# Kernel tuning notes

Hardware: AMD Instinct MI355X
Metric: run time of the kernel (lower is better)

## Reference

```python
import jax, jax.numpy as jnp
import numpy as np

N, D, M = 2048, 1024, 1024


def setup_inputs() -> dict:
    key = jax.random.key(0)
    ks = jax.random.split(key, 10)
    inputs = jax.random.normal(ks[0], (N, D), jnp.float32)
    # topological parent pointers: parent[t] > t; root (t=N-1) points to dummy slot N
    p = jax.random.randint(ks[1], (N,), jnp.arange(1, N + 1), N + 1)
    parent = jnp.where(jnp.arange(N) < N - 1, jnp.minimum(p, N - 1), N)
    s = 0.02
    Wioux = jax.random.normal(ks[2], (3 * M, D), jnp.float32) * s
    bioux = jax.random.normal(ks[3], (3 * M,), jnp.float32) * s
    Wiouh = jax.random.normal(ks[4], (3 * M, M), jnp.float32) * s
    biouh = jax.random.normal(ks[5], (3 * M,), jnp.float32) * s
    Wfx = jax.random.normal(ks[6], (M, D), jnp.float32) * s
    bfx = jax.random.normal(ks[7], (M,), jnp.float32) * s
    Wfh = jax.random.normal(ks[8], (M, M), jnp.float32) * s
    bfh = jax.random.normal(ks[9], (M,), jnp.float32) * s
    return dict(inputs=inputs, parent=parent, Wioux=Wioux, bioux=bioux,
                Wiouh=Wiouh, biouh=biouh, Wfx=Wfx, bfx=bfx, Wfh=Wfh, bfh=bfh)


def reference(inputs, parent, Wioux, bioux, Wiouh, biouh, Wfx, bfx, Wfh, bfh):
    # Child-Sum Tree-LSTM over nodes in topological order (children before parents).
    n, m = inputs.shape[0], Wfx.shape[0]
    ioux_all = inputs @ Wioux.T + bioux              # [N, 3M] self.ioux(inputs) for all nodes
    fx_all = inputs @ Wfx.T + bfx                    # [N, M]  self.fx(inputs) for all nodes
    fx_pad = jnp.concatenate([fx_all, jnp.zeros((1, m), fx_all.dtype)], axis=0)
    fxp = fx_pad[parent]                             # [N, M]  fx of each node's parent

    def step(carry, xs):
        h_sum, fc_sum = carry                        # [N+1, M] accumulated child sums
        t, iou_x, fxp_t, p = xs
        iou = iou_x + h_sum[t] @ Wiouh.T + biouh     # ioux(x) + iouh(child_h_sum)
        i, o, u = jnp.split(iou, 3)
        i, o, u = jax.nn.sigmoid(i), jax.nn.sigmoid(o), jnp.tanh(u)
        c = i * u + fc_sum[t]                        # i*u + sum_k f_k * c_k
        h = o * jnp.tanh(c)
        # forget gate for this node as a child of its parent: sigmoid(fh(h) + fx(x_parent))
        f = jax.nn.sigmoid(h @ Wfh.T + bfh + fxp_t)
        return (h_sum.at[p].add(h), fc_sum.at[p].add(f * c)), (c, h)

    init = (jnp.zeros((n + 1, m), inputs.dtype), jnp.zeros((n + 1, m), inputs.dtype))
    _, (cs, hs) = jax.lax.scan(step, init,
                               (jnp.arange(n), ioux_all, fxp, parent))
    # root is the last node in topological order; torch returns (c, h) each [1, mem_dim]
    return cs[-1:], hs[-1:]
```

## Files before the change

kernel.cpp:

```cpp
#include <hip/hip_runtime.h>

#define NN 2048
#define MD 1024
#define NOUT 4096
#define GBLK 256
#define GTHR 512
#define CAP 1024

typedef __attribute__((ext_vector_type(8))) short short8;
typedef __attribute__((ext_vector_type(4))) float f4;

__device__ __forceinline__ unsigned short f2bf(float f) {
  unsigned u = __float_as_uint(f);
  u += 0x7fffu + ((u >> 16) & 1u);
  return (unsigned short)(u >> 16);
}
__device__ __forceinline__ uint4 pack8(f4 a, f4 b) {
  uint4 r;
  r.x = f2bf(a[0]) | ((unsigned)f2bf(a[1]) << 16);
  r.y = f2bf(a[2]) | ((unsigned)f2bf(a[3]) << 16);
  r.z = f2bf(b[0]) | ((unsigned)f2bf(b[1]) << 16);
  r.w = f2bf(b[2]) | ((unsigned)f2bf(b[3]) << 16);
  return r;
}
__device__ __forceinline__ float blo(unsigned u) { return __uint_as_float(u << 16); }
__device__ __forceinline__ float bhi(unsigned u) { return __uint_as_float(u & 0xffff0000u); }
__device__ __forceinline__ float sigm(float x) { return 1.0f / (1.0f + __expf(-x)); }
__device__ __forceinline__ float tanh_(float x) { return 1.0f - 2.0f / (1.0f + __expf(2.0f * x)); }

__global__ __launch_bounds__(256) void cvt_bf16_kernel(const float* __restrict__ s,
                                                       unsigned short* __restrict__ d, int n4) {
  int i = blockIdx.x * 256 + threadIdx.x;
  if (i < n4) {
    f4 v = *((const f4*)s + i);
    unsigned lo = f2bf(v[0]) | ((unsigned)f2bf(v[1]) << 16);
    unsigned hi = f2bf(v[2]) | ((unsigned)f2bf(v[3]) << 16);
    uint2 r; r.x = lo; r.y = hi;
    *((uint2*)d + i) = r;
  }
}

__global__ __launch_bounds__(1024) void prep_kernel(const int* __restrict__ parent,
                                                    int2* __restrict__ meta,
                                                    int* __restrict__ doff_g,
                                                    int* __restrict__ maxd_out,
                                                    int* __restrict__ flags,
                                                    const float* __restrict__ bioux,
                                                    const float* __restrict__ biouh,
                                                    const float* __restrict__ bfx,
                                                    const float* __restrict__ bfh,
                                                    float* __restrict__ biasC) {
  __shared__ int s_anc[NN], s_dep[NN];
  __shared__ int s_t1[NN + 2], s_t2[NN + 2];
  __shared__ int s_poff[NN + 2], s_cur[NN + 2];
  __shared__ int s_ordp[NN], s_nord[NN];
  __shared__ int s_doff[NN + 2];
  __shared__ int s_sc[NN], s_sc2[NN];
  __shared__ int s_wsum[17];
  __shared__ int s_maxd;
  const int tid = threadIdx.x;

  if (tid == 0) s_maxd = 0;
  for (int i = tid; i < GBLK + 64; i += 1024) flags[i] = 0;
  for (int i = tid; i < NOUT; i += 1024)
    biasC[i] = (i < 3072) ? (bioux[i] + biouh[i]) : (bfx[i - 3072] + bfh[i - 3072]);
  for (int t = tid; t < NN; t += 1024) {
    bool root = (t == NN - 1);
    s_anc[t] = root ? t : parent[t];
    s_dep[t] = root ? 0 : 1;
  }
  __syncthreads();
  for (int it = 0; it < 11; ++it) {
    for (int t = tid; t < NN; t += 1024) { int a = s_anc[t]; s_t1[t] = s_dep[t] + s_dep[a]; s_t2[t] = s_anc[a]; }
    __syncthreads();
    for (int t = tid; t < NN; t += 1024) { s_dep[t] = s_t1[t]; s_anc[t] = s_t2[t]; }
    __syncthreads();
  }
  for (int t = tid; t < NN; t += 1024) atomicMax(&s_maxd, s_dep[t]);

  for (int i = tid; i < NN + 2; i += 1024) s_t2[i] = 0;
  __syncthreads();
  for (int t = tid; t < NN; t += 1024) atomicAdd(&s_t2[parent[t]], 1);
  __syncthreads();
  {
    const int L = NN + 2;
    int* src = s_t2; int* dst = s_t1;
    for (int o = 1; o < L; o <<= 1) {
      for (int i = tid; i < L; i += 1024) dst[i] = src[i] + ((i >= o) ? src[i - o] : 0);
      __syncthreads();
      int* tmp = src; src = dst; dst = tmp;
    }
    for (int i = tid; i < L; i += 1024) { int v = (i ? src[i - 1] : 0); s_poff[i] = v; s_cur[i] = v; }
    __syncthreads();
    for (int t = tid; t < NN; t += 1024) {
      int pos = atomicAdd(&s_cur[parent[t]], 1);
      s_ordp[pos] = t;
    }
    __syncthreads();
    for (int p = tid; p < NN + 1; p += 1024) {
      int b = s_poff[p], e = s_poff[p + 1];
      for (int i = b + 1; i < e; ++i) {
        int v = s_ordp[i], j = i - 1;
        while (j >= b && s_ordp[j] > v) { s_ordp[j + 1] = s_ordp[j]; --j; }
        s_ordp[j + 1] = v;
      }
    }
    __syncthreads();
  }

  for (int i = tid; i < NN + 2; i += 1024) s_t2[i] = 0;
  __syncthreads();
  for (int t = tid; t < NN; t += 1024) atomicAdd(&s_t2[s_dep[t]], 1);
  __syncthreads();
  {
    const int L = NN + 1;
    int* src = s_t2; int* dst = s_t1;
    for (int o = 1; o < L; o <<= 1) {
      for (int i = tid; i < L; i += 1024) dst[i] = src[i] + ((i >= o) ? src[i - o] : 0);
      __syncthreads();
      int* tmp = src; src = dst; dst = tmp;
    }
    for (int i = tid; i < L + 1; i += 1024) s_doff[i] = (i ? src[i - 1] : 0);
    __syncthreads();
  }

  const int maxd = s_maxd;
  if (tid == 0) s_nord[0] = NN - 1;
  __syncthreads();
  for (int d = 0; d < maxd; ++d) {
    const int lbeg = s_doff[d], lend = s_doff[d + 1];
    const int nd = lend - lbeg;
    if (nd <= 1024) {
      int t = -1, v = 0;
      if (tid < nd) { t = s_nord[lbeg + tid]; v = s_poff[t + 1] - s_poff[t]; }
      #pragma unroll
      for (int o = 1; o < 64; o <<= 1) {
        int u = __shfl_up(v, (unsigned)o, 64);
        if ((tid & 63) >= o) v += u;
      }
      if ((tid & 63) == 63) s_wsum[tid >> 6] = v;
      __syncthreads();
      if (tid < 16) {
        int w = s_wsum[tid];
        #pragma unroll
        for (int o = 1; o < 16; o <<= 1) {
          int u = __shfl_up(w, (unsigned)o, 16);
          if (tid >= o) w += u;
        }
        s_wsum[tid] = w;
      }
      __syncthreads();
      if (tid < nd) {
        int incl = v + ((tid >> 6) ? s_wsum[(tid >> 6) - 1] : 0);
        int cnti = s_poff[t + 1] - s_poff[t];
        int crel = incl - cnti;
        meta[lbeg + tid] = make_int2(t, (crel << 16) | cnti);
        for (int j = 0; j < cnti; ++j) s_nord[lend + crel + j] = s_ordp[s_poff[t] + j];
      }
      __syncthreads();
    } else {
      for (int i = tid; i < nd; i += 1024) { int t2 = s_nord[lbeg + i]; s_sc[i] = s_poff[t2 + 1] - s_poff[t2]; }
      __syncthreads();
      for (int o = 1; o < nd; o <<= 1) {
        for (int i = tid; i < nd; i += 1024) s_sc2[i] = s_sc[i] + ((i >= o) ? s_sc[i - o] : 0);
        __syncthreads();
        for (int i = tid; i < nd; i += 1024) s_sc[i] = s_sc2[i];
        __syncthreads();
      }
      for (int i = tid; i < nd; i += 1024) {
        int t2 = s_nord[lbeg + i];
        int cnti = s_poff[t2 + 1] - s_poff[t2];
        int crel = s_sc[i] - cnti;
        meta[lbeg + i] = make_int2(t2, (crel << 16) | cnti);
        for (int j = 0; j < cnti; ++j) s_nord[lend + crel + j] = s_ordp[s_poff[t2] + j];
      }
      __syncthreads();
    }
  }
  {
    const int lbeg = s_doff[maxd], lend = s_doff[maxd + 1];
    for (int i = lbeg + tid; i < lend; i += 1024)
      meta[i] = make_int2(s_nord[i], 0);
  }
  for (int i = tid; i <= maxd + 1; i += 1024) doff_g[i] = s_doff[i];
  if (tid == 0) *maxd_out = maxd;
}

__global__ __launch_bounds__(256) void pregemm_kernel(const unsigned short* __restrict__ Xb,
                                                      const unsigned short* __restrict__ Wb,
                                                      unsigned short* __restrict__ XWb,
                                                      const float* __restrict__ biasC) {
  __shared__ alignas(16) unsigned short ldsA[64 * 40];
  __shared__ alignas(16) unsigned short ldsB[64 * 40];
  const int xcd = blockIdx.x & 7;
  const int w = blockIdx.x >> 3;
  const int tn = xcd * 8 + (w & 7);
  const int tm = w >> 3;
  const int m0 = tm * 64, n0 = tn * 64;
  const int tid = threadIdx.x;
  const int lane = tid & 63;
  const int wave = tid >> 6;
  const int wr = wave >> 1, wc = wave & 1;
  f4 acc[2][2] = {};
  const int sr = tid >> 2;
  const int sc = (tid & 3) << 3;
  const unsigned short* agp = Xb + (size_t)(m0 + sr) * MD + sc;
  const unsigned short* bgp = Wb + (size_t)(n0 + sr) * MD + sc;
  const int lr = lane & 15;
  const int kq = (lane >> 4) << 3;

  for (int k0 = 0; k0 < MD; k0 += 32) {
    uint4 av = *(const uint4*)(agp + k0);
    uint4 bv = *(const uint4*)(bgp + k0);
    __syncthreads();
    *(uint4*)&ldsA[sr * 40 + sc] = av;
    *(uint4*)&ldsB[sr * 40 + sc] = bv;
    __syncthreads();
    short8 a0 = *(const short8*)&ldsA[(wr * 32 + lr) * 40 + kq];
    short8 a1 = *(const short8*)&ldsA[(wr * 32 + 16 + lr) * 40 + kq];
    short8 b0 = *(const short8*)&ldsB[(wc * 32 + lr) * 40 + kq];
    short8 b1 = *(const short8*)&ldsB[(wc * 32 + 16 + lr) * 40 + kq];
    acc[0][0] = __builtin_amdgcn_mfma_f32_16x16x32_bf16(a0, b0, acc[0][0], 0, 0, 0);
    acc[0][1] = __builtin_amdgcn_mfma_f32_16x16x32_bf16(a0, b1, acc[0][1], 0, 0, 0);
    acc[1][0] = __builtin_amdgcn_mfma_f32_16x16x32_bf16(a1, b0, acc[1][0], 0, 0, 0);
    acc[1][1] = __builtin_amdgcn_mfma_f32_16x16x32_bf16(a1, b1, acc[1][1], 0, 0, 0);
  }
  for (int r = 0; r < 2; ++r)
    for (int c = 0; c < 2; ++c)
      for (int q = 0; q < 4; ++q) {
        const int row = m0 + wr * 32 + r * 16 + (lane >> 4) * 4 + q;
        const int col = n0 + wc * 32 + c * 16 + lr;
        const float v = acc[r][c][q] + biasC[col];
        const int g = col >> 10, cj = col & 1023;
        XWb[((size_t)(cj >> 2) * NN + row) * 16 + (g << 2) + (cj & 3)] = f2bf(v);
      }
}

struct RP {
  const int2* meta;
  const int* doff;
  const int* maxd;
  const unsigned short* XWb;
  unsigned short* G2;
  float* CbB;
  unsigned short* Hb;
  const float* Wiouh;
  const float* Wfh;
  float* out;
  int* flags;
};

__device__ __forceinline__ void grid_barrier(int* flags, int step) {
  asm volatile("s_waitcnt vmcnt(0)" ::: "memory");
  __syncthreads();
  int* epoch = flags + GBLK;
  if (blockIdx.x == 0) {
    if (threadIdx.x < 64) {
      if (threadIdx.x == 0)
        __hip_atomic_store(&flags[0], step, __ATOMIC_RELAXED, __HIP_MEMORY_SCOPE_AGENT);
      const int base = threadIdx.x << 2;
      for (;;) {
        int a = __hip_atomic_load(&flags[base + 0], __ATOMIC_RELAXED, __HIP_MEMORY_SCOPE_AGENT);
        int b = __hip_atomic_load(&flags[base + 1], __ATOMIC_RELAXED, __HIP_MEMORY_SCOPE_AGENT);
        int c = __hip_atomic_load(&flags[base + 2], __ATOMIC_RELAXED, __HIP_MEMORY_SCOPE_AGENT);
        int d = __hip_atomic_load(&flags[base + 3], __ATOMIC_RELAXED, __HIP_MEMORY_SCOPE_AGENT);
        if (__all(a >= step && b >= step && c >= step && d >= step)) break;
        __builtin_amdgcn_s_sleep(1);
      }
      if (threadIdx.x == 0)
        __hip_atomic_store(epoch, step, __ATOMIC_RELAXED, __HIP_MEMORY_SCOPE_AGENT);
    }
  } else if (threadIdx.x == 0) {
    __hip_atomic_store(&flags[blockIdx.x], step, __ATOMIC_RELAXED, __HIP_MEMORY_SCOPE_AGENT);
    while (__hip_atomic_load(epoch, __ATOMIC_RELAXED, __HIP_MEMORY_SCOPE_AGENT) < step)
      __builtin_amdgcn_s_sleep(1);
  }
  __syncthreads();
  asm volatile("" ::: "memory");
}

#define GSTEP(A, KB)                                                                     \
  {                                                                                      \
    short8 bfrag = *(const short8*)(wb0 + ((((KB << 2) + kq) ^ swz) << 3));              \
    if ((KB) & 1) ao = __builtin_amdgcn_mfma_f32_16x16x32_bf16(A, bfrag, ao, 0, 0, 0);   \
    else          ae = __builtin_amdgcn_mfma_f32_16x16x32_bf16(A, bfrag, ae, 0, 0, 0);   \
    if ((KB) + 8 < 32) A = *(const short8*)(ap + (((KB) + 8) << 5));                     \
  }

__global__ __launch_bounds__(GTHR) void recur_kernel(RP p) {
  __shared__ alignas(16) unsigned short ldsW[16 * MD];
  __shared__ alignas(16) unsigned short G2L[CAP * 16];
  __shared__ alignas(16) float CbL[2 * CAP * 4];
  __shared__ int2 ldsMeta[NN];
  __shared__ int ldsDoff[NN + 2];
  const int tid = threadIdx.x;
  const int bid = blockIdx.x;
  const int lane = tid & 63;
  const int wave = tid >> 6;
  const int strip = (bid & 7) * 32 + (bid >> 3);
  const int s4 = strip << 2;

  for (int idx = tid; idx < 16 * 128; idx += GTHR) {
    int j = idx >> 7, kc = idx & 127;
    int g = j >> 2, col = s4 + (j & 3);
    const float* src = (g < 3) ? (p.Wiouh + (size_t)(g * MD + col) * MD)
                               : (p.Wfh + (size_t)col * MD);
    f4 lo = *(const f4*)(src + (kc << 3));
    f4 hi = *(const f4*)(src + (kc << 3) + 4);
    *(uint4*)(ldsW + j * MD + ((kc ^ (j & 7)) << 3)) = pack8(lo, hi);
  }
  const int maxd = *p.maxd;
  for (int i = tid; i < NN; i += GTHR) ldsMeta[i] = p.meta[i];
  for (int i = tid; i <= maxd + 1; i += GTHR) ldsDoff[i] = p.doff[i];
  __syncthreads();

  const unsigned short* xwb = p.XWb + (size_t)strip * NN * 16;
  unsigned short* G2g = p.G2 + (size_t)bid * NN * 16;
  float* CbBg = p.CbB + (size_t)bid * NN * 4;
  const int chalf = tid & 1;

  for (int d = maxd; d >= 0; --d) {
    const int lbeg = ldsDoff[d], lend = ldsDoff[d + 1];
    const int nd = lend - lbeg;
    float* cbw = CbL + (size_t)(d & 1) * CAP * 4;
    const float* cbr = CbL + (size_t)((d + 1) & 1) * CAP * 4;

    for (int ii = tid >> 1; ii < nd; ii += GTHR / 2) {
      const int2 mt = ldsMeta[lbeg + ii];
      const int t = mt.x, crel = mt.y >> 16, cnt = mt.y & 0xffff;
      const unsigned short* xwp = xwb + (size_t)t * 16;
      uint4 xa = *(const uint4*)xwp;
      uint4 xb = *(const uint4*)(xwp + 8);
      f4 gf; gf[0] = blo(xb.z); gf[1] = bhi(xb.z); gf[2] = blo(xb.w); gf[3] = bhi(xb.w);
      f4 gi = {0.f, 0.f, 0.f, 0.f}, go = gi, gu = gi, fc = gi;
      if (chalf == 0) {
        gi[0] = blo(xa.x); gi[1] = bhi(xa.x); gi[2] = blo(xa.y); gi[3] = bhi(xa.y);
        go[0] = blo(xa.z); go[1] = bhi(xa.z); go[2] = blo(xa.w); go[3] = bhi(xa.w);
        gu[0] = blo(xb.x); gu[1] = bhi(xb.x); gu[2] = blo(xb.y); gu[3] = bhi(xb.y);
      }
      for (int k = chalf; k < cnt; k += 2) {
        const int ci = crel + k;
        uint4 ga, gb; f4 cu;
        if (ci < CAP) {
          ga = *(const uint4*)(G2L + ci * 16);
          gb = *(const uint4*)(G2L + ci * 16 + 8);
          cu = *(const f4*)(cbr + ci * 4);
        } else {
          const unsigned short* g2 = G2g + (size_t)(lend + ci) * 16;
          ga = *(const uint4*)(g2);
          gb = *(const uint4*)(g2 + 8);
          cu = *(const f4*)(CbBg + (size_t)(lend + ci) * 4);
        }
        gi[0] += blo(ga.x); gi[1] += bhi(ga.x); gi[2] += blo(ga.y); gi[3] += bhi(ga.y);
        go[0] += blo(ga.z); go[1] += bhi(ga.z); go[2] += blo(ga.w); go[3] += bhi(ga.w);
        gu[0] += blo(gb.x); gu[1] += bhi(gb.x); gu[2] += blo(gb.y); gu[3] += bhi(gb.y);
        f4 gff; gff[0] = blo(gb.z); gff[1] = bhi(gb.z); gff[2] = blo(gb.w); gff[3] = bhi(gb.w);
        #pragma unroll
        for (int q = 0; q < 4; ++q) fc[q] += sigm(gff[q] + gf[q]) * cu[q];
      }
      #pragma unroll
      for (int q = 0; q < 4; ++q) {
        gi[q] += __shfl_xor(gi[q], 1);
        go[q] += __shfl_xor(go[q], 1);
        gu[q] += __shfl_xor(gu[q], 1);
        fc[q] += __shfl_xor(fc[q], 1);
      }
      if (chalf == 0) {
        f4 cv, hv;
        #pragma unroll
        for (int q = 0; q < 4; ++q) {
          float c0 = sigm(gi[q]) * tanh_(gu[q]) + fc[q];
          cv[q] = c0;
          hv[q] = sigm(go[q]) * tanh_(c0);
        }
        if (ii < CAP) *(f4*)(cbw + ii * 4) = cv;
        else          *(f4*)(CbBg + (size_t)(lbeg + ii) * 4) = cv;
        unsigned long long hp =
            (unsigned long long)f2bf(hv[0]) |
            ((unsigned long long)f2bf(hv[1]) << 16) |
            ((unsigned long long)f2bf(hv[2]) << 32) |
            ((unsigned long long)f2bf(hv[3]) << 48);
        __hip_atomic_store((unsigned long long*)(p.Hb + (size_t)t * MD + s4),
                           hp, __ATOMIC_RELAXED, __HIP_MEMORY_SCOPE_AGENT);
        if (t == NN - 1) {
          *(f4*)(p.out + s4) = cv;
          *(f4*)(p.out + MD + s4) = hv;
        }
      }
    }
    if (d == 0) break;

    grid_barrier(p.flags, maxd - d + 1);

    if (d > 0) {
      const int lbeg2 = ldsDoff[d - 1];
      const int nd2 = lbeg - lbeg2;
      for (int q2 = tid; q2 < nd2; q2 += GTHR) {
        unsigned v = *(const unsigned*)(xwb + (size_t)ldsMeta[lbeg2 + q2].x * 16);
        asm volatile("" :: "v"(v));
      }
    }

    {
      const int ntr = (nd + 15) >> 4;
      const int lr = lane & 15;
      const int kq = lane >> 4;
      const int swz = lr & 7;
      const unsigned short* wb0 = ldsW + lr * MD;
      for (int rt = wave; rt < ntr; rt += GTHR / 64) {
        const int r = (rt << 4) + lr;
        const int pos = lbeg + ((r < nd) ? r : 0);
        const int node = ldsMeta[pos].x;
        const unsigned short* ap = p.Hb + (size_t)node * MD + (kq << 3);
        short8 A0 = *(const short8*)(ap);
        short8 A1 = *(const short8*)(ap + 32);
        short8 A2 = *(const short8*)(ap + 64);
        short8 A3 = *(const short8*)(ap + 96);
        short8 A4 = *(const short8*)(ap + 128);
        short8 A5 = *(const short8*)(ap + 160);
        short8 A6 = *(const short8*)(ap + 192);
        short8 A7 = *(const short8*)(ap + 224);
        f4 ae = {0.f, 0.f, 0.f, 0.f}, ao = {0.f, 0.f, 0.f, 0.f};
        GSTEP(A0, 0)  GSTEP(A1, 1)  GSTEP(A2, 2)  GSTEP(A3, 3)
        GSTEP(A4, 4)  GSTEP(A5, 5)  GSTEP(A6, 6)  GSTEP(A7, 7)
        GSTEP(A0, 8)  GSTEP(A1, 9)  GSTEP(A2, 10) GSTEP(A3, 11)
        GSTEP(A4, 12) GSTEP(A5, 13) GSTEP(A6, 14) GSTEP(A7, 15)
        GSTEP(A0, 16) GSTEP(A1, 17) GSTEP(A2, 18) GSTEP(A3, 19)
        GSTEP(A4, 20) GSTEP(A5, 21) GSTEP(A6, 22) GSTEP(A7, 23)
        GSTEP(A0, 24) GSTEP(A1, 25) GSTEP(A2, 26) GSTEP(A3, 27)
        GSTEP(A4, 28) GSTEP(A5, 29) GSTEP(A6, 30) GSTEP(A7, 31)
        const int rb = (rt << 4) + (kq << 2);
        #pragma unroll
        for (int q = 0; q < 4; ++q) {
          const int rr = rb + q;
          if (rr < nd) {
            unsigned short v = f2bf(ae[q] + ao[q]);
            if (rr < CAP) G2L[rr * 16 + lr] = v;
            else          G2g[(size_t)(lbeg + rr) * 16 + lr] = v;
          }
        }
      }
    }
    __syncthreads();
  }
}

extern "C" void kernel_launch(void* const* d_in, const int* in_sizes, int n_in,
                              void* d_out, int out_size, void* d_ws, size_t ws_size,
                              hipStream_t stream) {
  const float* X     = (const float*)d_in[0];
  const int*   parent= (const int*)d_in[1];
  const float* Wioux = (const float*)d_in[2];
  const float* bioux = (const float*)d_in[3];
  const float* Wiouh = (const float*)d_in[4];
  const float* biouh = (const float*)d_in[5];
  const float* Wfx   = (const float*)d_in[6];
  const float* bfx   = (const float*)d_in[7];
  const float* Wfh   = (const float*)d_in[8];
  const float* bfh   = (const float*)d_in[9];
  float* out = (float*)d_out;

  char* ws = (char*)d_ws;
  size_t o = 0;
  auto alloc = [&](size_t bytes) { size_t r = o; o += (bytes + 255) & ~(size_t)255; return r; };
  unsigned short* Xb   = (unsigned short*)(ws + alloc((size_t)NN * MD * 2));
  unsigned short* Wpre = (unsigned short*)(ws + alloc((size_t)NOUT * MD * 2));
  unsigned short* XWb  = (unsigned short*)(ws + alloc((size_t)GBLK * NN * 16 * 2));
  unsigned short* G2   = (unsigned short*)(ws + alloc((size_t)GBLK * NN * 16 * 2));
  float* CbB           = (float*)(ws + alloc((size_t)GBLK * NN * 4 * 4));
  unsigned short* Hb   = (unsigned short*)(ws + alloc((size_t)NN * MD * 2));
  float* biasC         = (float*)(ws + alloc((size_t)NOUT * 4));
  int2* meta           = (int2*)(ws + alloc((size_t)NN * 8));
  int* doff            = (int*)(ws + alloc((NN + 4) * 4));
  int* maxd            = (int*)(ws + alloc(256));
  int* flags           = (int*)(ws + alloc((GBLK + 64) * 4));

  {
    int n4;
    n4 = NN * MD / 4;
    cvt_bf16_kernel<<<(n4 + 255) / 256, 256, 0, stream>>>(X, Xb, n4);
    n4 = 3072 * MD / 4;
    cvt_bf16_kernel<<<(n4 + 255) / 256, 256, 0, stream>>>(Wioux, Wpre, n4);
    n4 = 1024 * MD / 4;
    cvt_bf16_kernel<<<(n4 + 255) / 256, 256, 0, stream>>>(Wfx, Wpre + (size_t)3072 * MD, n4);
  }

  prep_kernel<<<1, 1024, 0, stream>>>(parent, meta, doff, maxd, flags,
                                      bioux, biouh, bfx, bfh, biasC);

  pregemm_kernel<<<(NN / 64) * (NOUT / 64), 256, 0, stream>>>(Xb, Wpre, XWb, biasC);

  RP p;
  p.meta = meta; p.doff = doff; p.maxd = maxd;
  p.XWb = XWb; p.G2 = G2; p.CbB = CbB; p.Hb = Hb;
  p.Wiouh = Wiouh; p.Wfh = Wfh;
  p.out = out; p.flags = flags;
  void* args[] = {&p};
  hipLaunchCooperativeKernel((const void*)recur_kernel, dim3(GBLK), dim3(GTHR), args, 0, stream);

  (void)in_sizes; (void)n_in; (void)out_size; (void)ws_size;
}
```

Baseline: 352.5 us.

## Fuse tree prep and input GEMM into the cooperative recurrence kernel

Removes the separate prep_kernel, the weight bf16 conversions and pregemm_kernel. Block 0 of the cooperative kernel now builds the level schedule while every block computes its own strip of the input projection X·W from fp32 weights packed into LDS. One grid barrier then precedes the recurrence. The per-level XWb prefetch is moved ahead of the grid barrier. This cuts launch count and global round trips, but block 0 carries the serial prep work that all other blocks wait on at the first barrier, and the input GEMM now runs as a per-strip matrix-vector style pass.

```diff
diff --git a/kernel.cpp b/kernel.cpp
--- a/kernel.cpp
+++ b/kernel.cpp
@@ -6,6 +6,7 @@
 #define GBLK 256
 #define GTHR 512
 #define CAP 1024
+#define NTILES (NN / 16)
 
 typedef __attribute__((ext_vector_type(8))) short short8;
 typedef __attribute__((ext_vector_type(4))) float f4;
@@ -40,212 +41,24 @@
   }
 }
 
-__global__ __launch_bounds__(1024) void prep_kernel(const int* __restrict__ parent,
-                                                    int2* __restrict__ meta,
-                                                    int* __restrict__ doff_g,
-                                                    int* __restrict__ maxd_out,
-                                                    int* __restrict__ flags,
-                                                    const float* __restrict__ bioux,
-                                                    const float* __restrict__ biouh,
-                                                    const float* __restrict__ bfx,
-                                                    const float* __restrict__ bfh,
-                                                    float* __restrict__ biasC) {
-  __shared__ int s_anc[NN], s_dep[NN];
-  __shared__ int s_t1[NN + 2], s_t2[NN + 2];
-  __shared__ int s_poff[NN + 2], s_cur[NN + 2];
-  __shared__ int s_ordp[NN], s_nord[NN];
-  __shared__ int s_doff[NN + 2];
-  __shared__ int s_sc[NN], s_sc2[NN];
-  __shared__ int s_wsum[17];
-  __shared__ int s_maxd;
-  const int tid = threadIdx.x;
-
-  if (tid == 0) s_maxd = 0;
-  for (int i = tid; i < GBLK + 64; i += 1024) flags[i] = 0;
-  for (int i = tid; i < NOUT; i += 1024)
-    biasC[i] = (i < 3072) ? (bioux[i] + biouh[i]) : (bfx[i - 3072] + bfh[i - 3072]);
-  for (int t = tid; t < NN; t += 1024) {
-    bool root = (t == NN - 1);
-    s_anc[t] = root ? t : parent[t];
-    s_dep[t] = root ? 0 : 1;
-  }
-  __syncthreads();
-  for (int it = 0; it < 11; ++it) {
-    for (int t = tid; t < NN; t += 1024) { int a = s_anc[t]; s_t1[t] = s_dep[t] + s_dep[a]; s_t2[t] = s_anc[a]; }
-    __syncthreads();
-    for (int t = tid; t < NN; t += 1024) { s_dep[t] = s_t1[t]; s_anc[t] = s_t2[t]; }
-    __syncthreads();
-  }
-  for (int t = tid; t < NN; t += 1024) atomicMax(&s_maxd, s_dep[t]);
-
-  for (int i = tid; i < NN + 2; i += 1024) s_t2[i] = 0;
-  __syncthreads();
-  for (int t = tid; t < NN; t += 1024) atomicAdd(&s_t2[parent[t]], 1);
-  __syncthreads();
-  {
-    const int L = NN + 2;
-    int* src = s_t2; int* dst = s_t1;
-    for (int o = 1; o < L; o <<= 1) {
-      for (int i = tid; i < L; i += 1024) dst[i] = src[i] + ((i >= o) ? src[i - o] : 0);
-      __syncthreads();
-      int* tmp = src; src = dst; dst = tmp;
-    }
-    for (int i = tid; i < L; i += 1024) { int v = (i ? src[i - 1] : 0); s_poff[i] = v; s_cur[i] = v; }
-    __syncthreads();
-    for (int t = tid; t < NN; t += 1024) {
-      int pos = atomicAdd(&s_cur[parent[t]], 1);
-      s_ordp[pos] = t;
-    }
-    __syncthreads();
-    for (int p = tid; p < NN + 1; p += 1024) {
-      int b = s_poff[p], e = s_poff[p + 1];
-      for (int i = b + 1; i < e; ++i) {
-        int v = s_ordp[i], j = i - 1;
-        while (j >= b && s_ordp[j] > v) { s_ordp[j + 1] = s_ordp[j]; --j; }
-        s_ordp[j + 1] = v;
-      }
-    }
-    __syncthreads();
-  }
-
-  for (int i = tid; i < NN + 2; i += 1024) s_t2[i] = 0;
-  __syncthreads();
-  for (int t = tid; t < NN; t += 1024) atomicAdd(&s_t2[s_dep[t]], 1);
-  __syncthreads();
-  {
-    const int L = NN + 1;
-    int* src = s_t2; int* dst = s_t1;
-    for (int o = 1; o < L; o <<= 1) {
-      for (int i = tid; i < L; i += 1024) dst[i] = src[i] + ((i >= o) ? src[i - o] : 0);
-      __syncthreads();
-      int* tmp = src; src = dst; dst = tmp;
-    }
-    for (int i = tid; i < L + 1; i += 1024) s_doff[i] = (i ? src[i - 1] : 0);
-    __syncthreads();
-  }
-
-  const int maxd = s_maxd;
-  if (tid == 0) s_nord[0] = NN - 1;
-  __syncthreads();
-  for (int d = 0; d < maxd; ++d) {
-    const int lbeg = s_doff[d], lend = s_doff[d + 1];
-    const int nd = lend - lbeg;
-    if (nd <= 1024) {
-      int t = -1, v = 0;
-      if (tid < nd) { t = s_nord[lbeg + tid]; v = s_poff[t + 1] - s_poff[t]; }
-      #pragma unroll
-      for (int o = 1; o < 64; o <<= 1) {
-        int u = __shfl_up(v, (unsigned)o, 64);
-        if ((tid & 63) >= o) v += u;
-      }
-      if ((tid & 63) == 63) s_wsum[tid >> 6] = v;
-      __syncthreads();
-      if (tid < 16) {
-        int w = s_wsum[tid];
-        #pragma unroll
-        for (int o = 1; o < 16; o <<= 1) {
-          int u = __shfl_up(w, (unsigned)o, 16);
-          if (tid >= o) w += u;
-        }
-        s_wsum[tid] = w;
-      }
-      __syncthreads();
-      if (tid < nd) {
-        int incl = v + ((tid >> 6) ? s_wsum[(tid >> 6) - 1] : 0);
-        int cnti = s_poff[t + 1] - s_poff[t];
-        int crel = incl - cnti;
-        meta[lbeg + tid] = make_int2(t, (crel << 16) | cnti);
-        for (int j = 0; j < cnti; ++j) s_nord[lend + crel + j] = s_ordp[s_poff[t] + j];
-      }
-      __syncthreads();
-    } else {
-      for (int i = tid; i < nd; i += 1024) { int t2 = s_nord[lbeg + i]; s_sc[i] = s_poff[t2 + 1] - s_poff[t2]; }
-      __syncthreads();
-      for (int o = 1; o < nd; o <<= 1) {
-        for (int i = tid; i < nd; i += 1024) s_sc2[i] = s_sc[i] + ((i >= o) ? s_sc[i - o] : 0);
-        __syncthreads();
-        for (int i = tid; i < nd; i += 1024) s_sc[i] = s_sc2[i];
-        __syncthreads();
-      }
-      for (int i = tid; i < nd; i += 1024) {
-        int t2 = s_nord[lbeg + i];
-        int cnti = s_poff[t2 + 1] - s_poff[t2];
-        int crel = s_sc[i] - cnti;
-        meta[lbeg + i] = make_int2(t2, (crel << 16) | cnti);
-        for (int j = 0; j < cnti; ++j) s_nord[lend + crel + j] = s_ordp[s_poff[t2] + j];
-      }
-      __syncthreads();
-    }
-  }
-  {
-    const int lbeg = s_doff[maxd], lend = s_doff[maxd + 1];
-    for (int i = lbeg + tid; i < lend; i += 1024)
-      meta[i] = make_int2(s_nord[i], 0);
-  }
-  for (int i = tid; i <= maxd + 1; i += 1024) doff_g[i] = s_doff[i];
-  if (tid == 0) *maxd_out = maxd;
-}
-
-__global__ __launch_bounds__(256) void pregemm_kernel(const unsigned short* __restrict__ Xb,
-                                                      const unsigned short* __restrict__ Wb,
-                                                      unsigned short* __restrict__ XWb,
-                                                      const float* __restrict__ biasC) {
-  __shared__ alignas(16) unsigned short ldsA[64 * 40];
-  __shared__ alignas(16) unsigned short ldsB[64 * 40];
-  const int xcd = blockIdx.x & 7;
-  const int w = blockIdx.x >> 3;
-  const int tn = xcd * 8 + (w & 7);
-  const int tm = w >> 3;
-  const int m0 = tm * 64, n0 = tn * 64;
-  const int tid = threadIdx.x;
-  const int lane = tid & 63;
-  const int wave = tid >> 6;
-  const int wr = wave >> 1, wc = wave & 1;
-  f4 acc[2][2] = {};
-  const int sr = tid >> 2;
-  const int sc = (tid & 3) << 3;
-  const unsigned short* agp = Xb + (size_t)(m0 + sr) * MD + sc;
-  const unsigned short* bgp = Wb + (size_t)(n0 + sr) * MD + sc;
-  const int lr = lane & 15;
-  const int kq = (lane >> 4) << 3;
-
-  for (int k0 = 0; k0 < MD; k0 += 32) {
-    uint4 av = *(const uint4*)(agp + k0);
-    uint4 bv = *(const uint4*)(bgp + k0);
-    __syncthreads();
-    *(uint4*)&ldsA[sr * 40 + sc] = av;
-    *(uint4*)&ldsB[sr * 40 + sc] = bv;
-    __syncthreads();
-    short8 a0 = *(const short8*)&ldsA[(wr * 32 + lr) * 40 + kq];
-    short8 a1 = *(const short8*)&ldsA[(wr * 32 + 16 + lr) * 40 + kq];
-    short8 b0 = *(const short8*)&ldsB[(wc * 32 + lr) * 40 + kq];
-    short8 b1 = *(const short8*)&ldsB[(wc * 32 + 16 + lr) * 40 + kq];
-    acc[0][0] = __builtin_amdgcn_mfma_f32_16x16x32_bf16(a0, b0, acc[0][0], 0, 0, 0);
-    acc[0][1] = __builtin_amdgcn_mfma_f32_16x16x32_bf16(a0, b1, acc[0][1], 0, 0, 0);
-    acc[1][0] = __builtin_amdgcn_mfma_f32_16x16x32_bf16(a1, b0, acc[1][0], 0, 0, 0);
-    acc[1][1] = __builtin_amdgcn_mfma_f32_16x16x32_bf16(a1, b1, acc[1][1], 0, 0, 0);
-  }
-  for (int r = 0; r < 2; ++r)
-    for (int c = 0; c < 2; ++c)
-      for (int q = 0; q < 4; ++q) {
-        const int row = m0 + wr * 32 + r * 16 + (lane >> 4) * 4 + q;
-        const int col = n0 + wc * 32 + c * 16 + lr;
-        const float v = acc[r][c][q] + biasC[col];
-        const int g = col >> 10, cj = col & 1023;
-        XWb[((size_t)(cj >> 2) * NN + row) * 16 + (g << 2) + (cj & 3)] = f2bf(v);
-      }
-}
-
 struct RP {
-  const int2* meta;
-  const int* doff;
-  const int* maxd;
-  const unsigned short* XWb;
+  const int* parent;
+  const unsigned short* Xb;
+  const float* Wioux;
+  const float* bioux;
+  const float* biouh;
+  const float* Wfx;
+  const float* bfx;
+  const float* bfh;
+  const float* Wiouh;
+  const float* Wfh;
+  unsigned short* XWb;
+  int2* meta;
+  int* doff;
+  int* maxd;
   unsigned short* G2;
   float* CbB;
   unsigned short* Hb;
-  const float* Wiouh;
-  const float* Wfh;
   float* out;
   int* flags;
 };
@@ -287,12 +100,36 @@
     if ((KB) + 8 < 32) A = *(const short8*)(ap + (((KB) + 8) << 5));                     \
   }
 
-__global__ __launch_bounds__(GTHR) void recur_kernel(RP p) {
-  __shared__ alignas(16) unsigned short ldsW[16 * MD];
-  __shared__ alignas(16) unsigned short G2L[CAP * 16];
-  __shared__ alignas(16) float CbL[2 * CAP * 4];
-  __shared__ int2 ldsMeta[NN];
-  __shared__ int ldsDoff[NN + 2];
+#define GSTEP32                                          \
+  GSTEP(A0, 0)  GSTEP(A1, 1)  GSTEP(A2, 2)  GSTEP(A3, 3) \
+  GSTEP(A4, 4)  GSTEP(A5, 5)  GSTEP(A6, 6)  GSTEP(A7, 7) \
+  GSTEP(A0, 8)  GSTEP(A1, 9)  GSTEP(A2, 10) GSTEP(A3, 11)\
+  GSTEP(A4, 12) GSTEP(A5, 13) GSTEP(A6, 14) GSTEP(A7, 15)\
+  GSTEP(A0, 16) GSTEP(A1, 17) GSTEP(A2, 18) GSTEP(A3, 19)\
+  GSTEP(A4, 20) GSTEP(A5, 21) GSTEP(A6, 22) GSTEP(A7, 23)\
+  GSTEP(A0, 24) GSTEP(A1, 25) GSTEP(A2, 26) GSTEP(A3, 27)\
+  GSTEP(A4, 28) GSTEP(A5, 29) GSTEP(A6, 30) GSTEP(A7, 31)
+
+__global__ __launch_bounds__(GTHR) void fused_kernel(RP p) {
+  __shared__ union {
+    struct {
+      unsigned short W[16 * MD];
+      unsigned short G2[CAP * 16];
+      float Cb[2 * CAP * 4];
+      int2 meta[NN];
+      int doff[NN + 2];
+    } r;
+    struct {
+      int anc[NN], dep[NN];
+      int t1[NN + 2], t2[NN + 2];
+      int poff[NN + 2], cur[NN + 2];
+      int ordp[NN], nord[NN];
+      int doff[NN + 2];
+      int sc[NN], sc2[NN];
+      int wsum[8];
+      int maxd;
+    } pp;
+  } L;
   const int tid = threadIdx.x;
   const int bid = blockIdx.x;
   const int lane = tid & 63;
@@ -300,6 +137,181 @@
   const int strip = (bid & 7) * 32 + (bid >> 3);
   const int s4 = strip << 2;
 
+  if (bid == 0) {
+    auto& P = L.pp;
+    if (tid == 0) P.maxd = 0;
+    for (int t = tid; t < NN; t += GTHR) {
+      bool root = (t == NN - 1);
+      P.anc[t] = root ? t : p.parent[t];
+      P.dep[t] = root ? 0 : 1;
+    }
+    __syncthreads();
+    for (int it = 0; it < 11; ++it) {
+      for (int t = tid; t < NN; t += GTHR) { int a = P.anc[t]; P.t1[t] = P.dep[t] + P.dep[a]; P.t2[t] = P.anc[a]; }
+      __syncthreads();
+      for (int t = tid; t < NN; t += GTHR) { P.dep[t] = P.t1[t]; P.anc[t] = P.t2[t]; }
+      __syncthreads();
+    }
+    for (int t = tid; t < NN; t += GTHR) atomicMax(&P.maxd, P.dep[t]);
+
+    for (int i = tid; i < NN + 2; i += GTHR) P.t2[i] = 0;
+    __syncthreads();
+    for (int t = tid; t < NN; t += GTHR) atomicAdd(&P.t2[p.parent[t]], 1);
+    __syncthreads();
+    {
+      const int Lc = NN + 2;
+      int* src = P.t2; int* dst = P.t1;
+      for (int o = 1; o < Lc; o <<= 1) {
+        for (int i = tid; i < Lc; i += GTHR) dst[i] = src[i] + ((i >= o) ? src[i - o] : 0);
+        __syncthreads();
+        int* tmp = src; src = dst; dst = tmp;
+      }
+      for (int i = tid; i < Lc; i += GTHR) { int v = (i ? src[i - 1] : 0); P.poff[i] = v; P.cur[i] = v; }
+      __syncthreads();
+      for (int t = tid; t < NN; t += GTHR) {
+        int pos = atomicAdd(&P.cur[p.parent[t]], 1);
+        P.ordp[pos] = t;
+      }
+      __syncthreads();
+      for (int pr = tid; pr < NN + 1; pr += GTHR) {
+        int b = P.poff[pr], e = P.poff[pr + 1];
+        for (int i = b + 1; i < e; ++i) {
+          int v = P.ordp[i], j = i - 1;
+          while (j >= b && P.ordp[j] > v) { P.ordp[j + 1] = P.ordp[j]; --j; }
+          P.ordp[j + 1] = v;
+        }
+      }
+      __syncthreads();
+    }
+    for (int i = tid; i < NN + 2; i += GTHR) P.t2[i] = 0;
+    __syncthreads();
+    for (int t = tid; t < NN; t += GTHR) atomicAdd(&P.t2[P.dep[t]], 1);
+    __syncthreads();
+    {
+      const int Lc = NN + 1;
+      int* src = P.t2; int* dst = P.t1;
+      for (int o = 1; o < Lc; o <<= 1) {
+        for (int i = tid; i < Lc; i += GTHR) dst[i] = src[i] + ((i >= o) ? src[i - o] : 0);
+        __syncthreads();
+        int* tmp = src; src = dst; dst = tmp;
+      }
+      for (int i = tid; i < Lc + 1; i += GTHR) P.doff[i] = (i ? src[i - 1] : 0);
+      __syncthreads();
+    }
+    const int maxd = P.maxd;
+    if (tid == 0) P.nord[0] = NN - 1;
+    __syncthreads();
+    for (int d = 0; d < maxd; ++d) {
+      const int lbeg = P.doff[d], lend = P.doff[d + 1];
+      const int nd = lend - lbeg;
+      if (nd <= GTHR) {
+        int t = -1, v = 0;
+        if (tid < nd) { t = P.nord[lbeg + tid]; v = P.poff[t + 1] - P.poff[t]; }
+        #pragma unroll
+        for (int o = 1; o < 64; o <<= 1) {
+          int u = __shfl_up(v, (unsigned)o, 64);
+          if ((tid & 63) >= o) v += u;
+        }
+        if ((tid & 63) == 63) P.wsum[tid >> 6] = v;
+        __syncthreads();
+        if (tid < 8) {
+          int w = P.wsum[tid];
+          #pragma unroll
+          for (int o = 1; o < 8; o <<= 1) {
+            int u = __shfl_up(w, (unsigned)o, 8);
+            if (tid >= o) w += u;
+          }
+          P.wsum[tid] = w;
+        }
+        __syncthreads();
+        if (tid < nd) {
+          int incl = v + ((tid >> 6) ? P.wsum[(tid >> 6) - 1] : 0);
+          int cnti = P.poff[t + 1] - P.poff[t];
+          int crel = incl - cnti;
+          unsigned long long m = ((unsigned long long)(unsigned)((crel << 16) | cnti) << 32) | (unsigned)t;
+          __hip_atomic_store((unsigned long long*)&p.meta[lbeg + tid], m,
+                             __ATOMIC_RELAXED, __HIP_MEMORY_SCOPE_AGENT);
+          for (int j = 0; j < cnti; ++j) P.nord[lend + crel + j] = P.ordp[P.poff[t] + j];
+        }
+        __syncthreads();
+      } else {
+        for (int i = tid; i < nd; i += GTHR) { int t2v = P.nord[lbeg + i]; P.sc[i] = P.poff[t2v + 1] - P.poff[t2v]; }
+        __syncthreads();
+        for (int o = 1; o < nd; o <<= 1) {
+          for (int i = tid; i < nd; i += GTHR) P.sc2[i] = P.sc[i] + ((i >= o) ? P.sc[i - o] : 0);
+          __syncthreads();
+          for (int i = tid; i < nd; i += GTHR) P.sc[i] = P.sc2[i];
+          __syncthreads();
+        }
+        for (int i = tid; i < nd; i += GTHR) {
+          int t2v = P.nord[lbeg + i];
+          int cnti = P.poff[t2v + 1] - P.poff[t2v];
+          int crel = P.sc[i] - cnti;
+          unsigned long long m = ((unsigned long long)(unsigned)((crel << 16) | cnti) << 32) | (unsigned)t2v;
+          __hip_atomic_store((unsigned long long*)&p.meta[lbeg + i], m,
+                             __ATOMIC_RELAXED, __HIP_MEMORY_SCOPE_AGENT);
+          for (int j = 0; j < cnti; ++j) P.nord[lend + crel + j] = P.ordp[P.poff[t2v] + j];
+        }
+        __syncthreads();
+      }
+    }
+    {
+      const int lbeg = P.doff[maxd], lend = P.doff[maxd + 1];
+      for (int i = lbeg + tid; i < lend; i += GTHR) {
+        unsigned long long m = (unsigned long long)(unsigned)P.nord[i];
+        __hip_atomic_store((unsigned long long*)&p.meta[i], m,
+                           __ATOMIC_RELAXED, __HIP_MEMORY_SCOPE_AGENT);
+      }
+    }
+    for (int i = tid; i <= maxd + 1; i += GTHR)
+      __hip_atomic_store(&p.doff[i], P.doff[i], __ATOMIC_RELAXED, __HIP_MEMORY_SCOPE_AGENT);
+    if (tid == 0)
+      __hip_atomic_store(p.maxd, maxd, __ATOMIC_RELAXED, __HIP_MEMORY_SCOPE_AGENT);
+    __syncthreads();
+  }
+
+  for (int idx = tid; idx < 16 * 128; idx += GTHR) {
+    int j = idx >> 7, kc = idx & 127;
+    int g = j >> 2, col = s4 + (j & 3);
+    const float* src = (g < 3) ? (p.Wioux + (size_t)(g * MD + col) * MD)
+                               : (p.Wfx + (size_t)col * MD);
+    f4 lo = *(const f4*)(src + (kc << 3));
+    f4 hi = *(const f4*)(src + (kc << 3) + 4);
+    *(uint4*)(L.r.W + j * MD + ((kc ^ (j & 7)) << 3)) = pack8(lo, hi);
+  }
+  __syncthreads();
+  {
+    const int lr = lane & 15;
+    const int kq = lane >> 4;
+    const int swz = lr & 7;
+    const unsigned short* wb0 = L.r.W + lr * MD;
+    const int gg = lr >> 2, cc = s4 + (lr & 3);
+    const float bias = (gg < 3) ? (p.bioux[gg * MD + cc] + p.biouh[gg * MD + cc])
+                                : (p.bfx[cc] + p.bfh[cc]);
+    unsigned short* xwbw = p.XWb + (size_t)strip * NN * 16;
+    for (int rt = wave; rt < NTILES; rt += GTHR / 64) {
+      const int node = (rt << 4) + lr;
+      const unsigned short* ap = p.Xb + (size_t)node * MD + (kq << 3);
+      short8 A0 = *(const short8*)(ap);
+      short8 A1 = *(const short8*)(ap + 32);
+      short8 A2 = *(const short8*)(ap + 64);
+      short8 A3 = *(const short8*)(ap + 96);
+      short8 A4 = *(const short8*)(ap + 128);
+      short8 A5 = *(const short8*)(ap + 160);
+      short8 A6 = *(const short8*)(ap + 192);
+      short8 A7 = *(const short8*)(ap + 224);
+      f4 ae = {0.f, 0.f, 0.f, 0.f}, ao = {0.f, 0.f, 0.f, 0.f};
+      GSTEP32
+      const int rb = (rt << 4) + (kq << 2);
+      #pragma unroll
+      for (int q = 0; q < 4; ++q)
+        xwbw[(size_t)(rb + q) * 16 + lr] = f2bf(ae[q] + ao[q] + bias);
+    }
+  }
+
+  grid_barrier(p.flags, 1);
+
+  const int maxd = *p.maxd;
   for (int idx = tid; idx < 16 * 128; idx += GTHR) {
     int j = idx >> 7, kc = idx & 127;
     int g = j >> 2, col = s4 + (j & 3);
@@ -307,11 +319,10 @@
                                : (p.Wfh + (size_t)col * MD);
     f4 lo = *(const f4*)(src + (kc << 3));
     f4 hi = *(const f4*)(src + (kc << 3) + 4);
-    *(uint4*)(ldsW + j * MD + ((kc ^ (j & 7)) << 3)) = pack8(lo, hi);
-  }
-  const int maxd = *p.maxd;
-  for (int i = tid; i < NN; i += GTHR) ldsMeta[i] = p.meta[i];
-  for (int i = tid; i <= maxd + 1; i += GTHR) ldsDoff[i] = p.doff[i];
+    *(uint4*)(L.r.W + j * MD + ((kc ^ (j & 7)) << 3)) = pack8(lo, hi);
+  }
+  for (int i = tid; i < NN; i += GTHR) L.r.meta[i] = p.meta[i];
+  for (int i = tid; i <= maxd + 1; i += GTHR) L.r.doff[i] = p.doff[i];
   __syncthreads();
 
   const unsigned short* xwb = p.XWb + (size_t)strip * NN * 16;
@@ -320,13 +331,13 @@
   const int chalf = tid & 1;
 
   for (int d = maxd; d >= 0; --d) {
-    const int lbeg = ldsDoff[d], lend = ldsDoff[d + 1];
+    const int lbeg = L.r.doff[d], lend = L.r.doff[d + 1];
     const int nd = lend - lbeg;
-    float* cbw = CbL + (size_t)(d & 1) * CAP * 4;
-    const float* cbr = CbL + (size_t)((d + 1) & 1) * CAP * 4;
+    float* cbw = L.r.Cb + (size_t)(d & 1) * CAP * 4;
+    const float* cbr = L.r.Cb + (size_t)((d + 1) & 1) * CAP * 4;
 
     for (int ii = tid >> 1; ii < nd; ii += GTHR / 2) {
-      const int2 mt = ldsMeta[lbeg + ii];
+      const int2 mt = L.r.meta[lbeg + ii];
       const int t = mt.x, crel = mt.y >> 16, cnt = mt.y & 0xffff;
       const unsigned short* xwp = xwb + (size_t)t * 16;
       uint4 xa = *(const uint4*)xwp;
@@ -342,8 +353,8 @@
         const int ci = crel + k;
         uint4 ga, gb; f4 cu;
         if (ci < CAP) {
-          ga = *(const uint4*)(G2L + ci * 16);
-          gb = *(const uint4*)(G2L + ci * 16 + 8);
+          ga = *(const uint4*)(L.r.G2 + ci * 16);
+          gb = *(const uint4*)(L.r.G2 + ci * 16 + 8);
           cu = *(const f4*)(cbr + ci * 4);
         } else {
           const unsigned short* g2 = G2g + (size_t)(lend + ci) * 16;
@@ -390,27 +401,27 @@
     }
     if (d == 0) break;
 
-    grid_barrier(p.flags, maxd - d + 1);
-
-    if (d > 0) {
-      const int lbeg2 = ldsDoff[d - 1];
+    {
+      const int lbeg2 = L.r.doff[d - 1];
       const int nd2 = lbeg - lbeg2;
       for (int q2 = tid; q2 < nd2; q2 += GTHR) {
-        unsigned v = *(const unsigned*)(xwb + (size_t)ldsMeta[lbeg2 + q2].x * 16);
+        unsigned v = *(const unsigned*)(xwb + (size_t)L.r.meta[lbeg2 + q2].x * 16);
         asm volatile("" :: "v"(v));
       }
     }
+
+    grid_barrier(p.flags, maxd - d + 2);
 
     {
       const int ntr = (nd + 15) >> 4;
       const int lr = lane & 15;
       const int kq = lane >> 4;
       const int swz = lr & 7;
-      const unsigned short* wb0 = ldsW + lr * MD;
+      const unsigned short* wb0 = L.r.W + lr * MD;
       for (int rt = wave; rt < ntr; rt += GTHR / 64) {
         const int r = (rt << 4) + lr;
         const int pos = lbeg + ((r < nd) ? r : 0);
-        const int node = ldsMeta[pos].x;
+        const int node = L.r.meta[pos].x;
         const unsigned short* ap = p.Hb + (size_t)node * MD + (kq << 3);
         short8 A0 = *(const short8*)(ap);
         short8 A1 = *(const short8*)(ap + 32);
@@ -421,21 +432,14 @@
         short8 A6 = *(const short8*)(ap + 192);
         short8 A7 = *(const short8*)(ap + 224);
         f4 ae = {0.f, 0.f, 0.f, 0.f}, ao = {0.f, 0.f, 0.f, 0.f};
-        GSTEP(A0, 0)  GSTEP(A1, 1)  GSTEP(A2, 2)  GSTEP(A3, 3)
-        GSTEP(A4, 4)  GSTEP(A5, 5)  GSTEP(A6, 6)  GSTEP(A7, 7)
-        GSTEP(A0, 8)  GSTEP(A1, 9)  GSTEP(A2, 10) GSTEP(A3, 11)
-        GSTEP(A4, 12) GSTEP(A5, 13) GSTEP(A6, 14) GSTEP(A7, 15)
-        GSTEP(A0, 16) GSTEP(A1, 17) GSTEP(A2, 18) GSTEP(A3, 19)
-        GSTEP(A4, 20) GSTEP(A5, 21) GSTEP(A6, 22) GSTEP(A7, 23)
-        GSTEP(A0, 24) GSTEP(A1, 25) GSTEP(A2, 26) GSTEP(A3, 27)
-        GSTEP(A4, 28) GSTEP(A5, 29) GSTEP(A6, 30) GSTEP(A7, 31)
+        GSTEP32
         const int rb = (rt << 4) + (kq << 2);
         #pragma unroll
         for (int q = 0; q < 4; ++q) {
           const int rr = rb + q;
           if (rr < nd) {
             unsigned short v = f2bf(ae[q] + ao[q]);
-            if (rr < CAP) G2L[rr * 16 + lr] = v;
+            if (rr < CAP) L.r.G2[rr * 16 + lr] = v;
             else          G2g[(size_t)(lbeg + rr) * 16 + lr] = v;
           }
         }
@@ -464,39 +468,27 @@
   size_t o = 0;
   auto alloc = [&](size_t bytes) { size_t r = o; o += (bytes + 255) & ~(size_t)255; return r; };
   unsigned short* Xb   = (unsigned short*)(ws + alloc((size_t)NN * MD * 2));
-  unsigned short* Wpre = (unsigned short*)(ws + alloc((size_t)NOUT * MD * 2));
   unsigned short* XWb  = (unsigned short*)(ws + alloc((size_t)GBLK * NN * 16 * 2));
   unsigned short* G2   = (unsigned short*)(ws + alloc((size_t)GBLK * NN * 16 * 2));
   float* CbB           = (float*)(ws + alloc((size_t)GBLK * NN * 4 * 4));
   unsigned short* Hb   = (unsigned short*)(ws + alloc((size_t)NN * MD * 2));
-  float* biasC         = (float*)(ws + alloc((size_t)NOUT * 4));
   int2* meta           = (int2*)(ws + alloc((size_t)NN * 8));
   int* doff            = (int*)(ws + alloc((NN + 4) * 4));
   int* maxd            = (int*)(ws + alloc(256));
   int* flags           = (int*)(ws + alloc((GBLK + 64) * 4));
 
-  {
-    int n4;
-    n4 = NN * MD / 4;
-    cvt_bf16_kernel<<<(n4 + 255) / 256, 256, 0, stream>>>(X, Xb, n4);
-    n4 = 3072 * MD / 4;
-    cvt_bf16_kernel<<<(n4 + 255) / 256, 256, 0, stream>>>(Wioux, Wpre, n4);
-    n4 = 1024 * MD / 4;
-    cvt_bf16_kernel<<<(n4 + 255) / 256, 256, 0, stream>>>(Wfx, Wpre + (size_t)3072 * MD, n4);
-  }
-
-  prep_kernel<<<1, 1024, 0, stream>>>(parent, meta, doff, maxd, flags,
-                                      bioux, biouh, bfx, bfh, biasC);
-
-  pregemm_kernel<<<(NN / 64) * (NOUT / 64), 256, 0, stream>>>(Xb, Wpre, XWb, biasC);
+  cvt_bf16_kernel<<<(NN * MD / 4 + 255) / 256, 256, 0, stream>>>(X, Xb, NN * MD / 4);
+  hipMemsetAsync(flags, 0, (GBLK + 64) * 4, stream);
 
   RP p;
-  p.meta = meta; p.doff = doff; p.maxd = maxd;
-  p.XWb = XWb; p.G2 = G2; p.CbB = CbB; p.Hb = Hb;
+  p.parent = parent; p.Xb = Xb;
+  p.Wioux = Wioux; p.bioux = bioux; p.biouh = biouh;
+  p.Wfx = Wfx; p.bfx = bfx; p.bfh = bfh;
   p.Wiouh = Wiouh; p.Wfh = Wfh;
-  p.out = out; p.flags = flags;
+  p.XWb = XWb; p.meta = meta; p.doff = doff; p.maxd = maxd;
+  p.G2 = G2; p.CbB = CbB; p.Hb = Hb; p.out = out; p.flags = flags;
   void* args[] = {&p};
-  hipLaunchCooperativeKernel((const void*)recur_kernel, dim3(GBLK), dim3(GTHR), args, 0, stream);
+  hipLaunchCooperativeKernel((const void*)fused_kernel, dim3(GBLK), dim3(GTHR), args, 0, stream);
 
   (void)in_sizes; (void)n_in; (void)out_size; (void)ws_size;
 }
```

New measurement: 421.0 us. 1.19x slower.
